# Optimization experiments

Measured on AMD Instinct MI355X. Metric: run time of the kernel, lower is better.

Reference implementation:

```python
import math
import jax, jax.numpy as jnp
import numpy as np

N, DIN, DOUT = 32768, 1024, 1024
C = 1.0            # ball curvature c (k = -c)
MIN_NORM = 1e-15
EPS_PROJ = 4e-3    # geoopt float32 boundary eps


def _safe_norm(x):
    # sqrt of clipped sum-of-squares: finite value and finite grad at 0
    return jnp.sqrt(jnp.clip(jnp.sum(x * x, axis=-1, keepdims=True), MIN_NORM))


def _artanh(u):
    return jnp.arctanh(jnp.clip(u, -1.0 + 1e-5, 1.0 - 1e-5))


def _project(x, c):
    norm = _safe_norm(x)
    maxnorm = (1.0 - EPS_PROJ) / jnp.sqrt(c)
    return jnp.where(norm > maxnorm, x / norm * maxnorm, x)


def _mobius_matvec(W, x, c):
    sqc = jnp.sqrt(c)
    x_norm = _safe_norm(x)                       # [N,1]
    mx = x @ W.T                                 # [N,DOUT]
    mx_norm = _safe_norm(mx)                     # [N,1]
    res = jnp.tanh(mx_norm / x_norm * _artanh(sqc * x_norm)) * mx / (mx_norm * sqc)
    zero = jnp.all(mx == 0, axis=-1, keepdims=True)
    return jnp.where(zero, jnp.zeros((), x.dtype), res)


def _expmap0(u, c):
    sqc = jnp.sqrt(c)
    u_norm = _safe_norm(u)
    return jnp.tanh(sqc * u_norm) * u / (sqc * u_norm)


def _mobius_add(x, y, c):
    x2 = jnp.sum(x * x, axis=-1, keepdims=True)
    y2 = jnp.sum(y * y, axis=-1, keepdims=True)
    xy = jnp.sum(x * y, axis=-1, keepdims=True)
    num = (1.0 + 2.0 * c * xy + c * y2) * x + (1.0 - c * x2) * y
    denom = 1.0 + 2.0 * c * xy + c * c * x2 * y2
    return num / jnp.clip(denom, MIN_NORM)


def setup_inputs() -> dict:
    key = jax.random.key(0)
    kx, kw, kb = jax.random.split(key, 3)
    x = jax.random.normal(kx, (N, DIN), jnp.float32)
    # place points strictly inside the unit Poincare ball
    x = x / (jnp.linalg.norm(x, axis=-1, keepdims=True) + 1.0) * 0.7
    limit = math.sqrt(2.0) * math.sqrt(6.0 / (DIN + DOUT))  # xavier_uniform gain=sqrt(2)
    weight = jax.random.uniform(kw, (DOUT, DIN), jnp.float32, -limit, limit)
    bias = 0.01 * jax.random.normal(kb, (DOUT,), jnp.float32)
    return {"x": x, "weight": weight, "bias": bias}


def reference(x, weight, bias) -> jnp.ndarray:
    c = jnp.float32(C)
    res = _mobius_matvec(weight, x, c)           # dropout=0 / eval: weight used as-is
    res = _project(res, c)
    hyp_bias = _project(_expmap0(bias[None, :], c), c)
    res = _project(_mobius_add(res, hyp_bias, c), c)
    return res
```

## Files before the change

kernel.cpp:

```cpp
#include <hip/hip_runtime.h>
#include <hip/hip_bf16.h>
#include <cmath>

#define NROWS 32768
#define DIN   1024
#define DOUT  1024
#define BM    64
#define BK    32
#define NKT   (DIN / BK)
#define MAXNORM 0.996f
#define XPAD  40

typedef __attribute__((ext_vector_type(8))) __bf16 bf16x8;
typedef __attribute__((ext_vector_type(4))) float  f32x4;

__device__ __forceinline__ void gload16(const void* g, void* l) {
    __builtin_amdgcn_global_load_lds(
        (const __attribute__((address_space(1))) void*)g,
        (__attribute__((address_space(3))) void*)l, 16, 0, 0);
}

__device__ __forceinline__ unsigned pack2bf(float a, float b) {
    union { unsigned u; __bf16 h[2]; } p;
    p.h[0] = (__bf16)a; p.h[1] = (__bf16)b;
    return p.u;
}

__global__ void conv_w_kernel(const float* __restrict__ Wf, __bf16* __restrict__ Wb) {
    int cid = blockIdx.x * blockDim.x + threadIdx.x;
    int q   = cid & 3;
    int n   = (cid >> 2) & (DOUT - 1);
    int kt  = cid >> 12;
    int k0  = kt * BK + ((q ^ ((n >> 1) & 3)) << 3);
    const float* src = Wf + (size_t)n * DIN + k0;
    f32x4 v0 = *(const f32x4*)src;
    f32x4 v1 = *(const f32x4*)(src + 4);
    uint4 o;
    o.x = pack2bf(v0[0], v0[1]); o.y = pack2bf(v0[2], v0[3]);
    o.z = pack2bf(v1[0], v1[1]); o.w = pack2bf(v1[2], v1[3]);
    *(uint4*)((char*)Wb + (size_t)cid * 16) = o;
}

template<bool WBF>
__global__ __launch_bounds__(512, 2) void hyp_kernel(
    const float* __restrict__ X,
    const float* __restrict__ Wf,
    const __bf16* __restrict__ Wb,
    const float* __restrict__ bias,
    float* __restrict__ out)
{
    __shared__ __align__(16) __bf16 Wt[2][DOUT * BK];
    __shared__ __align__(16) __bf16 Xt[2][BM * XPAD];
    __shared__ float hbs[DOUT];
    __shared__ float redq[BM][8];
    __shared__ float redd[BM][8];
    __shared__ float xsqs[BM];
    __shared__ float fco[BM][2];
    __shared__ float bred[8];

    const int tid  = threadIdx.x;
    const int lane = tid & 63;
    const int wid  = tid >> 6;
    const int l15  = lane & 15;
    const int l4   = lane >> 4;
    const int row0 = blockIdx.x * BM;

    const int xr = tid >> 3;
    const int xk = (tid & 7) * 4;
    const float* xp = X + (size_t)(row0 + xr) * DIN + xk;
    float xsq = 0.f;

    f32x4 acc[4][8];
    #pragma unroll
    for (int m = 0; m < 4; m++)
        #pragma unroll
        for (int nt = 0; nt < 8; nt++)
            acc[m][nt] = (f32x4){0.f, 0.f, 0.f, 0.f};

    auto STAGE = [&](int buf, int kt) {
        if (kt < NKT) {
            if constexpr (WBF) {
                #pragma unroll
                for (int j = 0; j < 8; j++) {
                    int c = (j << 9) + tid;
                    gload16((const char*)Wb + (((size_t)kt << 12) + c) * 16,
                            (char*)(&Wt[buf][0]) + (((j << 9) + (wid << 6)) << 4));
                }
            } else {
                #pragma unroll
                for (int j = 0; j < 8; j++) {
                    int c = (j << 9) + tid;
                    int q = c & 3, n = c >> 2;
                    int k0 = kt * BK + ((q ^ ((n >> 1) & 3)) << 3);
                    const float* src = Wf + (size_t)n * DIN + k0;
                    f32x4 v0 = *(const f32x4*)src;
                    f32x4 v1 = *(const f32x4*)(src + 4);
                    uint4 o;
                    o.x = pack2bf(v0[0], v0[1]); o.y = pack2bf(v0[2], v0[3]);
                    o.z = pack2bf(v1[0], v1[1]); o.w = pack2bf(v1[2], v1[3]);
                    *(uint4*)((char*)(&Wt[buf][0]) + c * 16) = o;
                }
            }
            f32x4 xv = *(const f32x4*)(xp + kt * BK);
            xsq += xv[0]*xv[0] + xv[1]*xv[1] + xv[2]*xv[2] + xv[3]*xv[3];
            uint2 pk;
            pk.x = pack2bf(xv[0], xv[1]);
            pk.y = pack2bf(xv[2], xv[3]);
            *(uint2*)((char*)(&Xt[buf][0]) + xr * (XPAD * 2) + xk * 2) = pk;
        }
    };

    STAGE(0, 0);

    float b0 = bias[tid], b1 = bias[tid + 512];
    float bs = b0 * b0 + b1 * b1;
    #pragma unroll
    for (int m = 1; m < 64; m <<= 1) bs += __shfl_xor(bs, m);
    if (lane == 0) bred[wid] = bs;
    __syncthreads();
    float tot = 0.f;
    #pragma unroll
    for (int i = 0; i < 8; i++) tot += bred[i];
    const float bnorm = sqrtf(fmaxf(tot, 1e-15f));
    const float bth   = tanhf(bnorm);
    float sc0 = bth / bnorm;
    float hn  = bth;
    if (hn > MAXNORM) { sc0 *= MAXNORM / hn; hn = MAXNORM; }
    hbs[tid]       = sc0 * b0;
    hbs[tid + 512] = sc0 * b1;
    const float y2c = hn * hn;
    __syncthreads();

    float hv[8];
    #pragma unroll
    for (int nt = 0; nt < 8; nt++) hv[nt] = hbs[(wid << 7) + (nt << 4) + l15];

    int cur = 0;
    for (int kt = 0; kt < NKT; kt++) {
        STAGE(cur ^ 1, kt + 1);
        const char* xb = (const char*)(&Xt[cur][0]);
        const char* wb = (const char*)(&Wt[cur][0]);
        bf16x8 a[4], b[8];
        #pragma unroll
        for (int m = 0; m < 4; m++)
            a[m] = *(const bf16x8*)(xb + ((m << 4) + l15) * (XPAD * 2) + (l4 << 4));
        #pragma unroll
        for (int nt = 0; nt < 8; nt++) {
            int n = (wid << 7) + (nt << 4) + l15;
            b[nt] = *(const bf16x8*)(wb + n * 64 + ((l4 ^ ((n >> 1) & 3)) << 4));
        }
        #pragma unroll
        for (int m = 0; m < 4; m++)
            #pragma unroll
            for (int nt = 0; nt < 8; nt++)
                acc[m][nt] = __builtin_amdgcn_mfma_f32_16x16x32_bf16(a[m], b[nt], acc[m][nt], 0, 0, 0);
        __syncthreads();
        cur ^= 1;
    }

    float xs = xsq;
    #pragma unroll
    for (int m = 1; m < 8; m <<= 1) xs += __shfl_xor(xs, m);
    if ((tid & 7) == 0) xsqs[xr] = xs;

    #pragma unroll
    for (int m = 0; m < 4; m++) {
        #pragma unroll
        for (int r = 0; r < 4; r++) {
            float s = 0.f, d = 0.f;
            #pragma unroll
            for (int nt = 0; nt < 8; nt++) {
                float v = acc[m][nt][r];
                s += v * v;
                d += v * hv[nt];
            }
            #pragma unroll
            for (int mm = 1; mm < 16; mm <<= 1) {
                s += __shfl_xor(s, mm);
                d += __shfl_xor(d, mm);
            }
            if (l15 == 0) {
                int rl = (m << 4) + (l4 << 2) + r;
                redq[rl][wid] = s;
                redd[rl][wid] = d;
            }
        }
    }
    __syncthreads();

    if (tid < BM) {
        int r = tid;
        float sq = 0.f, dt = 0.f;
        #pragma unroll
        for (int w = 0; w < 8; w++) { sq += redq[r][w]; dt += redd[r][w]; }
        float sx     = xsqs[r];
        float xnorm  = sqrtf(fmaxf(sx, 1e-15f));
        float mxnorm = sqrtf(fmaxf(sq, 1e-15f));
        float u  = fminf(xnorm, 1.f - 1e-5f);
        float tv = tanhf(mxnorm / xnorm * atanhf(u));
        float rn = fminf(tv, MAXNORM);
        float s  = rn / mxnorm;
        float xy = s * dt;
        float x2 = rn * rn;
        float Am = 1.f + 2.f * xy + y2c;
        float Bm = 1.f - x2;
        float Dm = fmaxf(1.f + 2.f * xy + x2 * y2c, 1e-15f);
        float g1 = Am * s / Dm;
        float g2 = Bm / Dm;
        float osq   = g1 * g1 * sq + 2.f * g1 * g2 * dt + g2 * g2 * y2c;
        float onorm = sqrtf(fmaxf(osq, 1e-15f));
        float psc   = onorm > MAXNORM ? MAXNORM / onorm : 1.f;
        fco[r][0] = g1 * psc;
        fco[r][1] = g2 * psc;
    }
    __syncthreads();

    #pragma unroll
    for (int m = 0; m < 4; m++) {
        #pragma unroll
        for (int r = 0; r < 4; r++) {
            int rl = (m << 4) + (l4 << 2) + r;
            float F1 = fco[rl][0], F2 = fco[rl][1];
            float* orow = out + (size_t)(row0 + rl) * DOUT + (wid << 7);
            #pragma unroll
            for (int nt = 0; nt < 8; nt++)
                orow[(nt << 4) + l15] = F1 * acc[m][nt][r] + F2 * hv[nt];
        }
    }
}

extern "C" void kernel_launch(void* const* d_in, const int* in_sizes, int n_in,
                              void* d_out, int out_size, void* d_ws, size_t ws_size,
                              hipStream_t stream) {
    const float* X    = (const float*)d_in[0];
    const float* W    = (const float*)d_in[1];
    const float* bias = (const float*)d_in[2];
    float* out = (float*)d_out;

    const size_t wb_bytes = (size_t)DOUT * DIN * 2;
    if (ws_size >= wb_bytes) {
        __bf16* Wb = (__bf16*)d_ws;
        conv_w_kernel<<<dim3(DOUT * DIN / (16 * 256) * 2), dim3(256), 0, stream>>>(W, Wb);
        hyp_kernel<true><<<dim3(NROWS / BM), dim3(512), 0, stream>>>(X, W, Wb, bias, out);
    } else {
        hyp_kernel<false><<<dim3(NROWS / BM), dim3(512), 0, stream>>>(X, W, nullptr, bias, out);
    }
}
```

Measured before the change: 135.4 us.

## Split weight tile into half-buffers with finer-grained async pipeline and manual waitcnt barriers

```diff
diff --git a/kernel.cpp b/kernel.cpp
--- a/kernel.cpp
+++ b/kernel.cpp
@@ -26,12 +26,21 @@
     return p.u;
 }
 
+#define WAITBAR(N) do {                                                   \
+    asm volatile("s_waitcnt vmcnt(" #N ") lgkmcnt(0)" ::: "memory");      \
+    __builtin_amdgcn_s_barrier();                                         \
+    __builtin_amdgcn_sched_barrier(0);                                    \
+} while (0)
+
 __global__ void conv_w_kernel(const float* __restrict__ Wf, __bf16* __restrict__ Wb) {
     int cid = blockIdx.x * blockDim.x + threadIdx.x;
-    int q   = cid & 3;
-    int n   = (cid >> 2) & (DOUT - 1);
-    int kt  = cid >> 12;
-    int k0  = kt * BK + ((q ^ ((n >> 1) & 3)) << 3);
+    int q  = cid & 3;
+    int r  = (cid >> 2) & 15;
+    int g2 = (cid >> 6) & 31;
+    int h  = (cid >> 11) & 1;
+    int kt = cid >> 12;
+    int n  = ((g2 << 1) + h) * 16 + r;
+    int k0 = kt * BK + ((q ^ ((r >> 1) & 3)) << 3);
     const float* src = Wf + (size_t)n * DIN + k0;
     f32x4 v0 = *(const f32x4*)src;
     f32x4 v1 = *(const f32x4*)(src + 4);
@@ -41,15 +50,14 @@
     *(uint4*)((char*)Wb + (size_t)cid * 16) = o;
 }
 
-template<bool WBF>
-__global__ __launch_bounds__(512, 2) void hyp_kernel(
+__global__ __launch_bounds__(512, 2) void hyp_kernel_pipe(
     const float* __restrict__ X,
-    const float* __restrict__ Wf,
     const __bf16* __restrict__ Wb,
     const float* __restrict__ bias,
     float* __restrict__ out)
 {
-    __shared__ __align__(16) __bf16 Wt[2][DOUT * BK];
+    __shared__ __align__(16) __bf16 WtA[2][512 * BK];
+    __shared__ __align__(16) __bf16 WtB[2][512 * BK];
     __shared__ __align__(16) __bf16 Xt[2][BM * XPAD];
     __shared__ float hbs[DOUT];
     __shared__ float redq[BM][8];
@@ -77,40 +85,69 @@
         for (int nt = 0; nt < 8; nt++)
             acc[m][nt] = (f32x4){0.f, 0.f, 0.f, 0.f};
 
-    auto STAGE = [&](int buf, int kt) {
-        if (kt < NKT) {
-            if constexpr (WBF) {
-                #pragma unroll
-                for (int j = 0; j < 8; j++) {
-                    int c = (j << 9) + tid;
-                    gload16((const char*)Wb + (((size_t)kt << 12) + c) * 16,
-                            (char*)(&Wt[buf][0]) + (((j << 9) + (wid << 6)) << 4));
-                }
-            } else {
-                #pragma unroll
-                for (int j = 0; j < 8; j++) {
-                    int c = (j << 9) + tid;
-                    int q = c & 3, n = c >> 2;
-                    int k0 = kt * BK + ((q ^ ((n >> 1) & 3)) << 3);
-                    const float* src = Wf + (size_t)n * DIN + k0;
-                    f32x4 v0 = *(const f32x4*)src;
-                    f32x4 v1 = *(const f32x4*)(src + 4);
-                    uint4 o;
-                    o.x = pack2bf(v0[0], v0[1]); o.y = pack2bf(v0[2], v0[3]);
-                    o.z = pack2bf(v1[0], v1[1]); o.w = pack2bf(v1[2], v1[3]);
-                    *(uint4*)((char*)(&Wt[buf][0]) + c * 16) = o;
-                }
-            }
-            f32x4 xv = *(const f32x4*)(xp + kt * BK);
-            xsq += xv[0]*xv[0] + xv[1]*xv[1] + xv[2]*xv[2] + xv[3]*xv[3];
-            uint2 pk;
-            pk.x = pack2bf(xv[0], xv[1]);
-            pk.y = pack2bf(xv[2], xv[3]);
-            *(uint2*)((char*)(&Xt[buf][0]) + xr * (XPAD * 2) + xk * 2) = pk;
-        }
-    };
-
-    STAGE(0, 0);
+    auto wsrc = [&](int kt, int h) -> const char* {
+        return (const char*)Wb + (((size_t)kt * 2 + h) << 15);
+    };
+    auto issueHalf = [&](const char* g, __bf16* lds) {
+        #pragma unroll
+        for (int j = 0; j < 4; j++) {
+            int c = (j << 9) + tid;
+            gload16(g + (size_t)c * 16,
+                    (char*)lds + (((j << 9) + (wid << 6)) << 4));
+        }
+    };
+
+    f32x4 xv;
+    auto xload  = [&](int kt) { xv = *(const f32x4*)(xp + kt * BK); };
+    auto xstage = [&](int dstbuf) {
+        xsq += xv[0]*xv[0] + xv[1]*xv[1] + xv[2]*xv[2] + xv[3]*xv[3];
+        uint2 pk;
+        pk.x = pack2bf(xv[0], xv[1]);
+        pk.y = pack2bf(xv[2], xv[3]);
+        *(uint2*)((char*)(&Xt[dstbuf][0]) + xr * (XPAD * 2) + xk * 2) = pk;
+    };
+
+    bf16x8 afr[4];
+    auto cmpA = [&](int buf) {
+        const char* xb = (const char*)(&Xt[buf][0]);
+        const char* wb = (const char*)(&WtA[buf][0]);
+        #pragma unroll
+        for (int m = 0; m < 4; m++)
+            afr[m] = *(const bf16x8*)(xb + ((m << 4) + l15) * (XPAD * 2) + (l4 << 4));
+        bf16x8 b[4];
+        #pragma unroll
+        for (int i = 0; i < 4; i++) {
+            int g2 = (wid << 2) + i;
+            b[i] = *(const bf16x8*)(wb + (((g2 << 6) + (l15 << 2) + (l4 ^ ((l15 >> 1) & 3))) << 4));
+        }
+        __builtin_amdgcn_s_setprio(1);
+        #pragma unroll
+        for (int i = 0; i < 4; i++)
+            #pragma unroll
+            for (int m = 0; m < 4; m++)
+                acc[m][i * 2] = __builtin_amdgcn_mfma_f32_16x16x32_bf16(afr[m], b[i], acc[m][i * 2], 0, 0, 0);
+        __builtin_amdgcn_s_setprio(0);
+    };
+    auto cmpB = [&](int buf) {
+        const char* wb = (const char*)(&WtB[buf][0]);
+        bf16x8 b[4];
+        #pragma unroll
+        for (int i = 0; i < 4; i++) {
+            int g2 = (wid << 2) + i;
+            b[i] = *(const bf16x8*)(wb + (((g2 << 6) + (l15 << 2) + (l4 ^ ((l15 >> 1) & 3))) << 4));
+        }
+        __builtin_amdgcn_s_setprio(1);
+        #pragma unroll
+        for (int i = 0; i < 4; i++)
+            #pragma unroll
+            for (int m = 0; m < 4; m++)
+                acc[m][i * 2 + 1] = __builtin_amdgcn_mfma_f32_16x16x32_bf16(afr[m], b[i], acc[m][i * 2 + 1], 0, 0, 0);
+        __builtin_amdgcn_s_setprio(0);
+    };
+
+    issueHalf(wsrc(0, 0), &WtA[0][0]);
+    issueHalf(wsrc(0, 1), &WtB[0][0]);
+    xload(0);
 
     float b0 = bias[tid], b1 = bias[tid + 512];
     float bs = b0 * b0 + b1 * b1;
@@ -135,28 +172,23 @@
     #pragma unroll
     for (int nt = 0; nt < 8; nt++) hv[nt] = hbs[(wid << 7) + (nt << 4) + l15];
 
-    int cur = 0;
-    for (int kt = 0; kt < NKT; kt++) {
-        STAGE(cur ^ 1, kt + 1);
-        const char* xb = (const char*)(&Xt[cur][0]);
-        const char* wb = (const char*)(&Wt[cur][0]);
-        bf16x8 a[4], b[8];
-        #pragma unroll
-        for (int m = 0; m < 4; m++)
-            a[m] = *(const bf16x8*)(xb + ((m << 4) + l15) * (XPAD * 2) + (l4 << 4));
-        #pragma unroll
-        for (int nt = 0; nt < 8; nt++) {
-            int n = (wid << 7) + (nt << 4) + l15;
-            b[nt] = *(const bf16x8*)(wb + n * 64 + ((l4 ^ ((n >> 1) & 3)) << 4));
-        }
-        #pragma unroll
-        for (int m = 0; m < 4; m++)
-            #pragma unroll
-            for (int nt = 0; nt < 8; nt++)
-                acc[m][nt] = __builtin_amdgcn_mfma_f32_16x16x32_bf16(a[m], b[nt], acc[m][nt], 0, 0, 0);
-        __syncthreads();
-        cur ^= 1;
-    }
+    xstage(0);
+    xload(1);
+
+    for (int kt = 0; kt < 30; kt += 2) {
+        issueHalf(wsrc(kt + 1, 0), &WtA[1][0]); WAITBAR(9); cmpA(0);
+        xstage(1); xload(kt + 2);
+        issueHalf(wsrc(kt + 1, 1), &WtB[1][0]); WAITBAR(9); cmpB(0);
+
+        issueHalf(wsrc(kt + 2, 0), &WtA[0][0]); WAITBAR(9); cmpA(1);
+        xstage(0); xload(kt + 3);
+        issueHalf(wsrc(kt + 2, 1), &WtB[0][0]); WAITBAR(9); cmpB(1);
+    }
+    issueHalf(wsrc(31, 0), &WtA[1][0]); WAITBAR(9); cmpA(0);
+    xstage(1);
+    issueHalf(wsrc(31, 1), &WtB[1][0]); WAITBAR(8); cmpB(0);
+    WAITBAR(4); cmpA(1);
+    WAITBAR(0); cmpB(1);
 
     float xs = xsq;
     #pragma unroll
@@ -229,6 +261,182 @@
     }
 }
 
+__global__ __launch_bounds__(512, 2) void hyp_kernel_basic(
+    const float* __restrict__ X,
+    const float* __restrict__ Wf,
+    const float* __restrict__ bias,
+    float* __restrict__ out)
+{
+    __shared__ __align__(16) __bf16 Wt[2][DOUT * BK];
+    __shared__ __align__(16) __bf16 Xt[2][BM * XPAD];
+    __shared__ float hbs[DOUT];
+    __shared__ float redq[BM][8];
+    __shared__ float redd[BM][8];
+    __shared__ float xsqs[BM];
+    __shared__ float fco[BM][2];
+    __shared__ float bred[8];
+
+    const int tid  = threadIdx.x;
+    const int lane = tid & 63;
+    const int wid  = tid >> 6;
+    const int l15  = lane & 15;
+    const int l4   = lane >> 4;
+    const int row0 = blockIdx.x * BM;
+    const int xr = tid >> 3;
+    const int xk = (tid & 7) * 4;
+    const float* xp = X + (size_t)(row0 + xr) * DIN + xk;
+    float xsq = 0.f;
+
+    f32x4 acc[4][8];
+    #pragma unroll
+    for (int m = 0; m < 4; m++)
+        #pragma unroll
+        for (int nt = 0; nt < 8; nt++)
+            acc[m][nt] = (f32x4){0.f, 0.f, 0.f, 0.f};
+
+    auto STAGE = [&](int buf, int kt) {
+        if (kt < NKT) {
+            #pragma unroll
+            for (int j = 0; j < 8; j++) {
+                int c = (j << 9) + tid;
+                int q = c & 3, n = c >> 2;
+                int k0 = kt * BK + ((q ^ ((n >> 1) & 3)) << 3);
+                const float* src = Wf + (size_t)n * DIN + k0;
+                f32x4 v0 = *(const f32x4*)src;
+                f32x4 v1 = *(const f32x4*)(src + 4);
+                uint4 o;
+                o.x = pack2bf(v0[0], v0[1]); o.y = pack2bf(v0[2], v0[3]);
+                o.z = pack2bf(v1[0], v1[1]); o.w = pack2bf(v1[2], v1[3]);
+                *(uint4*)((char*)(&Wt[buf][0]) + c * 16) = o;
+            }
+            f32x4 xv = *(const f32x4*)(xp + kt * BK);
+            xsq += xv[0]*xv[0] + xv[1]*xv[1] + xv[2]*xv[2] + xv[3]*xv[3];
+            uint2 pk;
+            pk.x = pack2bf(xv[0], xv[1]);
+            pk.y = pack2bf(xv[2], xv[3]);
+            *(uint2*)((char*)(&Xt[buf][0]) + xr * (XPAD * 2) + xk * 2) = pk;
+        }
+    };
+
+    STAGE(0, 0);
+
+    float b0 = bias[tid], b1 = bias[tid + 512];
+    float bs = b0 * b0 + b1 * b1;
+    #pragma unroll
+    for (int m = 1; m < 64; m <<= 1) bs += __shfl_xor(bs, m);
+    if (lane == 0) bred[wid] = bs;
+    __syncthreads();
+    float tot = 0.f;
+    #pragma unroll
+    for (int i = 0; i < 8; i++) tot += bred[i];
+    const float bnorm = sqrtf(fmaxf(tot, 1e-15f));
+    const float bth   = tanhf(bnorm);
+    float sc0 = bth / bnorm;
+    float hn  = bth;
+    if (hn > MAXNORM) { sc0 *= MAXNORM / hn; hn = MAXNORM; }
+    hbs[tid]       = sc0 * b0;
+    hbs[tid + 512] = sc0 * b1;
+    const float y2c = hn * hn;
+    __syncthreads();
+
+    float hv[8];
+    #pragma unroll
+    for (int nt = 0; nt < 8; nt++) hv[nt] = hbs[(wid << 7) + (nt << 4) + l15];
+
+    int cur = 0;
+    for (int kt = 0; kt < NKT; kt++) {
+        STAGE(cur ^ 1, kt + 1);
+        const char* xb = (const char*)(&Xt[cur][0]);
+        const char* wb = (const char*)(&Wt[cur][0]);
+        bf16x8 a[4], b[8];
+        #pragma unroll
+        for (int m = 0; m < 4; m++)
+            a[m] = *(const bf16x8*)(xb + ((m << 4) + l15) * (XPAD * 2) + (l4 << 4));
+        #pragma unroll
+        for (int nt = 0; nt < 8; nt++) {
+            int n = (wid << 7) + (nt << 4) + l15;
+            b[nt] = *(const bf16x8*)(wb + n * 64 + ((l4 ^ ((n >> 1) & 3)) << 4));
+        }
+        #pragma unroll
+        for (int m = 0; m < 4; m++)
+            #pragma unroll
+            for (int nt = 0; nt < 8; nt++)
+                acc[m][nt] = __builtin_amdgcn_mfma_f32_16x16x32_bf16(a[m], b[nt], acc[m][nt], 0, 0, 0);
+        __syncthreads();
+        cur ^= 1;
+    }
+
+    float xs = xsq;
+    #pragma unroll
+    for (int m = 1; m < 8; m <<= 1) xs += __shfl_xor(xs, m);
+    if ((tid & 7) == 0) xsqs[xr] = xs;
+
+    #pragma unroll
+    for (int m = 0; m < 4; m++) {
+        #pragma unroll
+        for (int r = 0; r < 4; r++) {
+            float s = 0.f, d = 0.f;
+            #pragma unroll
+            for (int nt = 0; nt < 8; nt++) {
+                float v = acc[m][nt][r];
+                s += v * v;
+                d += v * hv[nt];
+            }
+            #pragma unroll
+            for (int mm = 1; mm < 16; mm <<= 1) {
+                s += __shfl_xor(s, mm);
+                d += __shfl_xor(d, mm);
+            }
+            if (l15 == 0) {
+                int rl = (m << 4) + (l4 << 2) + r;
+                redq[rl][wid] = s;
+                redd[rl][wid] = d;
+            }
+        }
+    }
+    __syncthreads();
+
+    if (tid < BM) {
+        int r = tid;
+        float sq = 0.f, dt = 0.f;
+        #pragma unroll
+        for (int w = 0; w < 8; w++) { sq += redq[r][w]; dt += redd[r][w]; }
+        float sx     = xsqs[r];
+        float xnorm  = sqrtf(fmaxf(sx, 1e-15f));
+        float mxnorm = sqrtf(fmaxf(sq, 1e-15f));
+        float u  = fminf(xnorm, 1.f - 1e-5f);
+        float tv = tanhf(mxnorm / xnorm * atanhf(u));
+        float rn = fminf(tv, MAXNORM);
+        float s  = rn / mxnorm;
+        float xy = s * dt;
+        float x2 = rn * rn;
+        float Am = 1.f + 2.f * xy + y2c;
+        float Bm = 1.f - x2;
+        float Dm = fmaxf(1.f + 2.f * xy + x2 * y2c, 1e-15f);
+        float g1 = Am * s / Dm;
+        float g2 = Bm / Dm;
+        float osq   = g1 * g1 * sq + 2.f * g1 * g2 * dt + g2 * g2 * y2c;
+        float onorm = sqrtf(fmaxf(osq, 1e-15f));
+        float psc   = onorm > MAXNORM ? MAXNORM / onorm : 1.f;
+        fco[r][0] = g1 * psc;
+        fco[r][1] = g2 * psc;
+    }
+    __syncthreads();
+
+    #pragma unroll
+    for (int m = 0; m < 4; m++) {
+        #pragma unroll
+        for (int r = 0; r < 4; r++) {
+            int rl = (m << 4) + (l4 << 2) + r;
+            float F1 = fco[rl][0], F2 = fco[rl][1];
+            float* orow = out + (size_t)(row0 + rl) * DOUT + (wid << 7);
+            #pragma unroll
+            for (int nt = 0; nt < 8; nt++)
+                orow[(nt << 4) + l15] = F1 * acc[m][nt][r] + F2 * hv[nt];
+        }
+    }
+}
+
 extern "C" void kernel_launch(void* const* d_in, const int* in_sizes, int n_in,
                               void* d_out, int out_size, void* d_ws, size_t ws_size,
                               hipStream_t stream) {
@@ -240,9 +448,9 @@
     const size_t wb_bytes = (size_t)DOUT * DIN * 2;
     if (ws_size >= wb_bytes) {
         __bf16* Wb = (__bf16*)d_ws;
-        conv_w_kernel<<<dim3(DOUT * DIN / (16 * 256) * 2), dim3(256), 0, stream>>>(W, Wb);
-        hyp_kernel<true><<<dim3(NROWS / BM), dim3(512), 0, stream>>>(X, W, Wb, bias, out);
+        conv_w_kernel<<<dim3(512), dim3(256), 0, stream>>>(W, Wb);
+        hyp_kernel_pipe<<<dim3(NROWS / BM), dim3(512), 0, stream>>>(X, Wb, bias, out);
     } else {
-        hyp_kernel<false><<<dim3(NROWS / BM), dim3(512), 0, stream>>>(X, W, nullptr, bias, out);
-    }
-}
+        hyp_kernel_basic<<<dim3(NROWS / BM), dim3(512), 0, stream>>>(X, W, bias, out);
+    }
+}
```

Measured after the change: 121.7 us. 10.2% less time.
